# Optimization experiments

Measured on AMD Instinct MI355X. Metric: run time of the kernel, lower is better.

Reference implementation:

```python
import jax, jax.numpy as jnp
import numpy as np
from jax import lax

B, N, C, T = 32, 1000, 32, 24
K, F_CHEB, F_TIME = 3, 64, 64


def setup_inputs() -> dict:
    key = jax.random.key(0)
    ks = jax.random.split(key, 7)
    return {
        "x": jax.random.normal(ks[0], (B, N, C, T), dtype=jnp.float32),
        "cheb_T": jax.random.normal(ks[1], (K, N, N), dtype=jnp.float32) * (1.0 / np.sqrt(N)),
        "Theta": jax.random.normal(ks[2], (K, C, F_CHEB), dtype=jnp.float32) * 0.1,
        "time_w": jax.random.normal(ks[3], (F_TIME, F_CHEB, 1, 3), dtype=jnp.float32) * 0.05,
        "time_b": jax.random.normal(ks[4], (F_TIME,), dtype=jnp.float32) * 0.05,
        "res_w": jax.random.normal(ks[5], (F_TIME, C, 1, 1), dtype=jnp.float32) * 0.1,
        "res_b": jax.random.normal(ks[6], (F_TIME,), dtype=jnp.float32) * 0.05,
    }


def _conv2d(x, w, stride_t, pad_t):
    # x: [B, Cin, N, T] (NCHW with H=nodes, W=time), w: [Cout, Cin, kh, kw]
    return lax.conv_general_dilated(
        x, w, window_strides=(1, stride_t), padding=((0, 0), (pad_t, pad_t)),
        dimension_numbers=("NCHW", "OIHW", "NCHW"))


def reference(x, cheb_T, Theta, time_w, time_b, res_w, res_b):
    # ChebConv: rhs_k[b,n,c,t] = sum_m T_k[m,n] x[b,m,c,t]; out = sum_k rhs_k @ Theta_k
    # Fused over all timesteps and polynomial orders in one einsum.
    spatial = jax.nn.relu(
        jnp.einsum("knm,bmct,kcf->bnft", cheb_T, x, Theta))  # [B,N,F_cheb,T]
    # time conv over the T axis (kernel (1,3), pad (0,1), stride (1,1))
    h = spatial.transpose(0, 2, 1, 3)  # [B,F_cheb,N,T]
    tc = _conv2d(h, time_w, 1, 1) + time_b[None, :, None, None]
    tc = jnp.tanh(tc) * jax.nn.sigmoid(tc)  # wave-net gating
    # 1x1 residual conv on the raw input (Dropout output in source is unused)
    res = _conv2d(x.transpose(0, 2, 1, 3), res_w, 1, 0) + res_b[None, :, None, None]
    out = (res + tc).transpose(0, 2, 1, 3)  # [B,N,F_time,T]
    return out
```

## Files before the change

### kernel.cpp

```cpp
#include <hip/hip_runtime.h>
#include <math.h>

typedef __attribute__((ext_vector_type(4))) float f32x4;
typedef __attribute__((ext_vector_type(16))) float f32x16;
typedef __attribute__((ext_vector_type(8))) short s16x8;
typedef __attribute__((ext_vector_type(8))) unsigned short u16x8;
typedef __attribute__((ext_vector_type(4))) unsigned short u16x4;

#define NB 32
#define NN 1000
#define NT 24
#define NP 1024
#define TCN 768

#define GLOAD16(g, l) __builtin_amdgcn_global_load_lds( \
    (const __attribute__((address_space(1))) unsigned int*)(g), \
    (__attribute__((address_space(3))) unsigned int*)(l), 16, 0, 0)

__device__ __forceinline__ unsigned short f2bf(float f){
  union { float fv; unsigned int u; } v; v.fv = f;
  unsigned int r = v.u + 0x7FFFu + ((v.u >> 16) & 1u);
  return (unsigned short)(r >> 16);
}

__global__ void k0_cheb(const float* __restrict__ cheb, unsigned short* __restrict__ cbT){
  int idx = blockIdx.x * 256 + threadIdx.x;
  int base = idx << 2;
  int m = base & (NP - 1);
  int r = base >> 10;
  int n = r & (NP - 1);
  int k = r >> 10;
  u16x4 o = (u16x4){0,0,0,0};
  if (n < NN && m < NN){
    if (m + 3 < NN){
      f32x4 v = *(const f32x4*)(cheb + ((size_t)k*NN + n)*NN + m);
      o[0] = f2bf(v[0]); o[1] = f2bf(v[1]); o[2] = f2bf(v[2]); o[3] = f2bf(v[3]);
    } else {
      #pragma unroll
      for (int i = 0; i < 4; ++i)
        if (m + i < NN) o[i] = f2bf(cheb[((size_t)k*NN + n)*NN + m + i]);
    }
  }
  *(u16x4*)(cbT + base) = o;
}

__global__ __launch_bounds__(256) void k0_x(const float* __restrict__ x,
                     unsigned short* __restrict__ xbT, unsigned short* __restrict__ xt2){
  __shared__ unsigned short tile[64*770];
  const int b  = blockIdx.x >> 4;
  const int m0 = (blockIdx.x & 15) << 6;
  const int tid = threadIdx.x;
  for (int i = tid; i < 64*192; i += 256){
    int mi = i / 192, c4 = (i - mi*192) << 2;
    f32x4 v = (f32x4){0.f,0.f,0.f,0.f};
    if (m0 + mi < NN) v = *(const f32x4*)(x + (size_t)(b*NN + m0 + mi)*768 + c4);
    unsigned short* tp = tile + mi*770 + c4;
    tp[0] = f2bf(v[0]); tp[1] = f2bf(v[1]); tp[2] = f2bf(v[2]); tp[3] = f2bf(v[3]);
  }
  __syncthreads();
  {
    const int seg = tid & 7, r0 = tid >> 3;
    for (int rr = 0; rr < 768; rr += 32){
      int r = rr + r0;
      int t = r >> 5, c = r & 31, ct = c*24 + t;
      u16x8 v;
      #pragma unroll
      for (int e = 0; e < 8; ++e) v[e] = tile[(seg*8 + e)*770 + ct];
      *(u16x8*)(xbT + ((size_t)b*TCN + r)*NP + m0 + seg*8) = v;
    }
  }
  if (m0 < NN){
    int rows = NN - m0; if (rows > 64) rows = 64;
    for (int i = tid; i < rows*96; i += 256){
      int mi = i / 96, s = i - mi*96;
      u16x8 v;
      #pragma unroll
      for (int e = 0; e < 8; ++e){
        int r = s*8 + e; int t = r >> 5, c = r & 31;
        v[e] = tile[mi*770 + c*24 + t];
      }
      *(u16x8*)(xt2 + (size_t)(b*NN + m0 + mi)*TCN + s*8) = v;
    }
  }
}

__global__ void k0_w(const float* __restrict__ Theta, const float* __restrict__ tw,
                     const float* __restrict__ rw,
                     unsigned short* __restrict__ ThT, unsigned short* __restrict__ WtT,
                     unsigned short* __restrict__ rwT){
  int i = blockIdx.x * 256 + threadIdx.x;
  if (i < 64*96){
    int f = i / 96, kc = i - f*96;
    ThT[i] = f2bf(Theta[kc*64 + f]);
  }
  if (i < 64*192){
    int f = i / 192, kk = i - f*192;
    int dt = kk >> 6, fi = kk & 63;
    WtT[i] = f2bf(tw[(f*64 + fi)*3 + dt]);
  }
  if (i < 64*32){
    rwT[i] = f2bf(rw[i]);
  }
}

__global__ __launch_bounds__(256, 3) void k1_cheb_theta(
    const unsigned short* __restrict__ cbT,
    const unsigned short* __restrict__ xbT,
    const unsigned short* __restrict__ ThT,
    unsigned short* __restrict__ spa)
{
  __shared__ __align__(16) unsigned short smem[20480];

  int pB = blockIdx.x;
  int lb = (pB & 7) * 384 + (pB >> 3);
  const int tcb = lb % 6; lb /= 6;
  const int nt  = lb & 15;
  const int b   = lb >> 4;

  const int tid  = threadIdx.x;
  const int wid  = tid >> 6;
  const int lane = tid & 63;
  const int l31  = lane & 31;
  const int h    = lane >> 5;
  const int wr   = wid >> 1;
  const int wc   = wid & 1;

  const int rl4 = lane >> 2;
  const int swz = (((lane & 3) ^ ((rl4 >> 1) & 3)) << 3);
  const unsigned short* baseA = cbT + (size_t)(nt*64 + rl4)*NP + swz;
  const unsigned short* baseB = xbT + ((size_t)b*TCN + tcb*128 + rl4)*NP + swz;
  char* smc = (char*)smem;

  const int s_rd = (l31 >> 1) & 3;
  const int ch0 = ((h ^ s_rd) << 3);
  const int ch1 = (((2 + h) ^ s_rd) << 3);

  f32x16 acc[3][2];
  #pragma unroll
  for (int k = 0; k < 3; ++k)
    #pragma unroll
    for (int j = 0; j < 2; ++j)
      #pragma unroll
      for (int r = 0; r < 16; ++r) acc[k][j][r] = 0.f;

  const int rA  = wr*32 + l31;
  const int rB0 = wc*64 + l31;

  {
    #pragma unroll
    for (int q = 0; q < 5; ++q){
      const int g = wid*5 + q;
      if (g < 12){
        const int k = g >> 2, rg = g & 3;
        GLOAD16(baseA + (size_t)k*NP*NP + rg*16*NP, smc + k*4096 + rg*1024);
      } else {
        const int rg = g - 12;
        GLOAD16(baseB + (size_t)rg*16*NP, smc + 12288 + rg*1024);
      }
    }
  }
  __syncthreads();

  int cur = 0;
  for (int step = 0; step < 32; ++step){
    if (step < 31){
      const int so = (step + 1) << 5;
      const int bo = (cur ^ 1) * 20480;
      #pragma unroll
      for (int q = 0; q < 5; ++q){
        const int g = wid*5 + q;
        if (g < 12){
          const int k = g >> 2, rg = g & 3;
          GLOAD16(baseA + (size_t)k*NP*NP + rg*16*NP + so, smc + bo + k*4096 + rg*1024);
        } else {
          const int rg = g - 12;
          GLOAD16(baseB + (size_t)rg*16*NP + so, smc + bo + 12288 + rg*1024);
        }
      }
    }
    const unsigned short* sb = smem + cur*10240;
    #pragma unroll
    for (int ks = 0; ks < 2; ++ks){
      const int ch = ks ? ch1 : ch0;
      s16x8 bf0 = *(const s16x8*)(sb + 6144 + rB0*32 + ch);
      s16x8 bf1 = *(const s16x8*)(sb + 6144 + (rB0 + 32)*32 + ch);
      #pragma unroll
      for (int k = 0; k < 3; ++k){
        s16x8 af = *(const s16x8*)(sb + k*2048 + rA*32 + ch);
        acc[k][0] = __builtin_amdgcn_mfma_f32_32x32x16_bf16(af, bf0, acc[k][0], 0, 0, 0);
        acc[k][1] = __builtin_amdgcn_mfma_f32_32x32x16_bf16(af, bf1, acc[k][1], 0, 0, 0);
      }
    }
    __syncthreads();
    cur ^= 1;
  }

  s16x8 b2[3][2];
  const int fE = wc*32 + l31;
  #pragma unroll
  for (int ch = 0; ch < 3; ++ch)
    #pragma unroll
    for (int ks = 0; ks < 2; ++ks)
      b2[ch][ks] = *(const s16x8*)(ThT + fE*96 + ch*32 + ks*16 + h*8);

  unsigned short* yl = smem;
  const int rowE = wr*32 + l31;
  #pragma unroll
  for (int p = 0; p < 4; ++p){
    __syncthreads();
    if (wc == (p >> 1)){
      const int jj = p & 1;
      #pragma unroll
      for (int k = 0; k < 3; ++k)
        #pragma unroll
        for (int r = 0; r < 16; ++r){
          const int nl = wr*32 + (r & 3) + ((r >> 2) << 3) + (h << 2);
          const int kc = k*32 + l31;
          const int q  = kc >> 3;
          yl[nl*104 + (((q ^ (nl & 3)) << 3) | (kc & 7))] = f2bf(acc[k][jj][r]);
        }
    }
    __syncthreads();
    f32x16 a2c;
    #pragma unroll
    for (int r = 0; r < 16; ++r) a2c[r] = 0.f;
    #pragma unroll
    for (int ch = 0; ch < 3; ++ch)
      #pragma unroll
      for (int ks = 0; ks < 2; ++ks){
        const int q = ch*4 + ks*2 + h;
        s16x8 a2 = *(const s16x8*)(yl + rowE*104 + ((q ^ (rowE & 3)) << 3));
        a2c = __builtin_amdgcn_mfma_f32_32x32x16_bf16(a2, b2[ch][ks], a2c, 0, 0, 0);
      }
    const int t = tcb*4 + p;
    #pragma unroll
    for (int r = 0; r < 16; ++r){
      const int nl = wr*32 + (r & 3) + ((r >> 2) << 3) + (h << 2);
      const int n  = nt*64 + nl;
      if (n < NN)
        spa[((size_t)(b*NN + n)*NT + t)*64 + fE] = f2bf(fmaxf(a2c[r], 0.f));
    }
  }
}

__global__ __launch_bounds__(256, 2) void k2_out(
    const unsigned short* __restrict__ spa, const unsigned short* __restrict__ xt2,
    const unsigned short* __restrict__ WtT, const unsigned short* __restrict__ rwT,
    const float* __restrict__ tb, const float* __restrict__ rb,
    float* __restrict__ out)
{
  __shared__ __align__(16) unsigned short sst[36864];
  const unsigned short* spa_s = sst;
  const unsigned short* xt2_s = sst + 24576;

  const int c0   = blockIdx.x * 16;
  const int tid  = threadIdx.x;
  const int w    = tid >> 6;
  const int lane = tid & 63;
  const int l31  = lane & 31;
  const int h    = lane >> 5;
  char* smc = (char*)sst;

  const unsigned short* gs = spa + (size_t)c0 * 1536;
  const unsigned short* gx = xt2 + (size_t)c0 * 768;
  #pragma unroll
  for (int it = 0; it < 12; ++it){
    const int row = it*32 + (tid >> 3);
    const int sc  = (tid & 7) ^ (row & 7);
    GLOAD16(gs + (size_t)row*64 + sc*8, smc + it*4096 + w*1024);
  }
  #pragma unroll
  for (int it = 0; it < 6; ++it){
    const int row = it*64 + (tid >> 2);
    const int sc  = (tid & 3) ^ ((row >> 1) & 3);
    GLOAD16(gx + (size_t)row*32 + sc*8, smc + 49152 + it*4096 + w*1024);
  }
  __syncthreads();

  const float tb0v = tb[l31], tb1v = tb[32 + l31];
  const float rb0v = rb[l31], rb1v = rb[32 + l31];

  #pragma unroll
  for (int g = 0; g < 3; ++g){
    const int rbase = w*96 + g*32;
    const int r = rbase + l31;
    const int cell = r / 24;
    const int t = r - cell*24;

    f32x16 a0, a1, rs0, rs1;
    #pragma unroll
    for (int e = 0; e < 16; ++e){ a0[e]=0.f; a1[e]=0.f; rs0[e]=0.f; rs1[e]=0.f; }

    #pragma unroll
    for (int s = 0; s < 12; ++s){
      const int dt = s >> 2;
      const int tv = t + dt - 1;
      int ar = r + dt - 1;
      ar = ar < 0 ? 0 : (ar > 383 ? 383 : ar);
      const int cfi = ((s & 3) << 1) + h;
      s16x8 a = *(const s16x8*)(spa_s + (size_t)ar*64 + ((cfi ^ (ar & 7)) << 3));
      if (!((unsigned)tv < 24u)) a = (s16x8){0,0,0,0,0,0,0,0};
      s16x8 b0 = *(const s16x8*)(WtT + (size_t)l31*192 + s*16 + h*8);
      s16x8 b1 = *(const s16x8*)(WtT + (size_t)(32 + l31)*192 + s*16 + h*8);
      a0 = __builtin_amdgcn_mfma_f32_32x32x16_bf16(a, b0, a0, 0, 0, 0);
      a1 = __builtin_amdgcn_mfma_f32_32x32x16_bf16(a, b1, a1, 0, 0, 0);
    }
    #pragma unroll
    for (int s = 0; s < 2; ++s){
      const int cres = (s << 1) + h;
      s16x8 a = *(const s16x8*)(xt2_s + (size_t)r*32 + ((cres ^ ((r >> 1) & 3)) << 3));
      s16x8 b0 = *(const s16x8*)(rwT + (size_t)l31*32 + s*16 + h*8);
      s16x8 b1 = *(const s16x8*)(rwT + (size_t)(32 + l31)*32 + s*16 + h*8);
      rs0 = __builtin_amdgcn_mfma_f32_32x32x16_bf16(a, b0, rs0, 0, 0, 0);
      rs1 = __builtin_amdgcn_mfma_f32_32x32x16_bf16(a, b1, rs1, 0, 0, 0);
    }

    #pragma unroll
    for (int q = 0; q < 4; ++q){
      const int rq = rbase + q*8 + 4*h;
      const int cq = rq / 24;
      const int tq = rq - cq*24;
      f32x4 v0, v1;
      #pragma unroll
      for (int e = 0; e < 4; ++e){
        float z0 = a0[q*4 + e] + tb0v;
        float e0 = __expf(-z0);
        v0[e] = rs0[q*4 + e] + rb0v + (1.f - e0) * __builtin_amdgcn_rcpf(1.f + e0*e0);
        float z1 = a1[q*4 + e] + tb1v;
        float e1 = __expf(-z1);
        v1[e] = rs1[q*4 + e] + rb1v + (1.f - e1) * __builtin_amdgcn_rcpf(1.f + e1*e1);
      }
      *(f32x4*)(out + ((size_t)(c0 + cq)*64 + l31)*24 + tq)      = v0;
      *(f32x4*)(out + ((size_t)(c0 + cq)*64 + 32 + l31)*24 + tq) = v1;
    }
  }
}

extern "C" void kernel_launch(void* const* d_in, const int* in_sizes, int n_in,
                              void* d_out, int out_size, void* d_ws, size_t ws_size,
                              hipStream_t stream) {
  const float* x     = (const float*)d_in[0];
  const float* cheb  = (const float*)d_in[1];
  const float* Theta = (const float*)d_in[2];
  const float* tw    = (const float*)d_in[3];
  const float* tb    = (const float*)d_in[4];
  const float* rw    = (const float*)d_in[5];
  const float* rb    = (const float*)d_in[6];
  float* out = (float*)d_out;

  char* ws = (char*)d_ws;
  size_t off = 0;
  auto alloc = [&](size_t bytes) -> void* {
    void* p = ws + off;
    off += (bytes + 255) & ~(size_t)255;
    return p;
  };
  unsigned short* cbT = (unsigned short*)alloc((size_t)3*NP*NP*2);
  unsigned short* xbT = (unsigned short*)alloc((size_t)NB*TCN*NP*2);
  unsigned short* xt2 = (unsigned short*)alloc((size_t)NB*NN*TCN*2);
  unsigned short* spa = (unsigned short*)alloc((size_t)NB*NN*NT*64*2);
  unsigned short* ThT = (unsigned short*)alloc((size_t)64*96*2);
  unsigned short* WtT = (unsigned short*)alloc((size_t)64*192*2);
  unsigned short* rwT = (unsigned short*)alloc((size_t)64*32*2);

  hipLaunchKernelGGL(k0_cheb, dim3(3072), dim3(256), 0, stream, cheb, cbT);
  hipLaunchKernelGGL(k0_x,    dim3(512),  dim3(256), 0, stream, x, xbT, xt2);
  hipLaunchKernelGGL(k0_w,    dim3(48),   dim3(256), 0, stream, Theta, tw, rw, ThT, WtT, rwT);
  hipLaunchKernelGGL(k1_cheb_theta, dim3(32*16*6), dim3(256), 0, stream, cbT, xbT, ThT, spa);
  hipLaunchKernelGGL(k2_out,  dim3(2000), dim3(256), 0, stream, spa, xt2, WtT, rwT, tb, rb, out);
}
```

Before: 391.8 us.

## Triple-buffer k1 loads with explicit vmcnt waits and MFMA priority

Extends the k1 GEMM main loop from double to triple buffering in LDS, so loads are prefetched two steps ahead. The previous __syncthreads is replaced by explicit s_waitcnt vmcnt plus s_barrier, which lets one stage's loads stay in flight across the barrier. MFMAs are grouped after hoisting the A-fragment LDS reads and wrapped in s_setprio. The larger LDS footprint lowers the launch-bounds occupancy target from 3 to 2 blocks per CU, trading latency hiding from occupancy for deeper prefetch.

```diff
diff --git a/kernel.cpp b/kernel.cpp
--- a/kernel.cpp
+++ b/kernel.cpp
@@ -103,13 +103,13 @@
   }
 }
 
-__global__ __launch_bounds__(256, 3) void k1_cheb_theta(
+__global__ __launch_bounds__(256, 2) void k1_cheb_theta(
     const unsigned short* __restrict__ cbT,
     const unsigned short* __restrict__ xbT,
     const unsigned short* __restrict__ ThT,
     unsigned short* __restrict__ spa)
 {
-  __shared__ __align__(16) unsigned short smem[20480];
+  __shared__ __align__(16) unsigned short smem[30720];
 
   int pB = blockIdx.x;
   int lb = (pB & 7) * 384 + (pB >> 3);
@@ -146,53 +146,53 @@
   const int rA  = wr*32 + l31;
   const int rB0 = wc*64 + l31;
 
-  {
+  auto stage = [&](int step, int buf){
+    const int so = step << 5;
+    const int bo = buf * 20480;
     #pragma unroll
     for (int q = 0; q < 5; ++q){
       const int g = wid*5 + q;
       if (g < 12){
         const int k = g >> 2, rg = g & 3;
-        GLOAD16(baseA + (size_t)k*NP*NP + rg*16*NP, smc + k*4096 + rg*1024);
+        GLOAD16(baseA + (size_t)k*NP*NP + rg*16*NP + so, smc + bo + k*4096 + rg*1024);
       } else {
         const int rg = g - 12;
-        GLOAD16(baseB + (size_t)rg*16*NP, smc + 12288 + rg*1024);
+        GLOAD16(baseB + (size_t)rg*16*NP + so, smc + bo + 12288 + rg*1024);
       }
     }
-  }
-  __syncthreads();
-
-  int cur = 0;
+  };
+
+  stage(0, 0);
+  stage(1, 1);
+  asm volatile("s_waitcnt vmcnt(5)" ::: "memory");
+  __builtin_amdgcn_s_barrier();
+
+  int cur = 0, pre = 2;
   for (int step = 0; step < 32; ++step){
-    if (step < 31){
-      const int so = (step + 1) << 5;
-      const int bo = (cur ^ 1) * 20480;
-      #pragma unroll
-      for (int q = 0; q < 5; ++q){
-        const int g = wid*5 + q;
-        if (g < 12){
-          const int k = g >> 2, rg = g & 3;
-          GLOAD16(baseA + (size_t)k*NP*NP + rg*16*NP + so, smc + bo + k*4096 + rg*1024);
-        } else {
-          const int rg = g - 12;
-          GLOAD16(baseB + (size_t)rg*16*NP + so, smc + bo + 12288 + rg*1024);
-        }
-      }
-    }
+    if (step < 30) stage(step + 2, pre);
     const unsigned short* sb = smem + cur*10240;
     #pragma unroll
     for (int ks = 0; ks < 2; ++ks){
       const int ch = ks ? ch1 : ch0;
       s16x8 bf0 = *(const s16x8*)(sb + 6144 + rB0*32 + ch);
       s16x8 bf1 = *(const s16x8*)(sb + 6144 + (rB0 + 32)*32 + ch);
-      #pragma unroll
-      for (int k = 0; k < 3; ++k){
-        s16x8 af = *(const s16x8*)(sb + k*2048 + rA*32 + ch);
-        acc[k][0] = __builtin_amdgcn_mfma_f32_32x32x16_bf16(af, bf0, acc[k][0], 0, 0, 0);
-        acc[k][1] = __builtin_amdgcn_mfma_f32_32x32x16_bf16(af, bf1, acc[k][1], 0, 0, 0);
-      }
-    }
-    __syncthreads();
-    cur ^= 1;
+      s16x8 af0 = *(const s16x8*)(sb +        rA*32 + ch);
+      s16x8 af1 = *(const s16x8*)(sb + 2048 + rA*32 + ch);
+      s16x8 af2 = *(const s16x8*)(sb + 4096 + rA*32 + ch);
+      __builtin_amdgcn_s_setprio(1);
+      acc[0][0] = __builtin_amdgcn_mfma_f32_32x32x16_bf16(af0, bf0, acc[0][0], 0, 0, 0);
+      acc[0][1] = __builtin_amdgcn_mfma_f32_32x32x16_bf16(af0, bf1, acc[0][1], 0, 0, 0);
+      acc[1][0] = __builtin_amdgcn_mfma_f32_32x32x16_bf16(af1, bf0, acc[1][0], 0, 0, 0);
+      acc[1][1] = __builtin_amdgcn_mfma_f32_32x32x16_bf16(af1, bf1, acc[1][1], 0, 0, 0);
+      acc[2][0] = __builtin_amdgcn_mfma_f32_32x32x16_bf16(af2, bf0, acc[2][0], 0, 0, 0);
+      acc[2][1] = __builtin_amdgcn_mfma_f32_32x32x16_bf16(af2, bf1, acc[2][1], 0, 0, 0);
+      __builtin_amdgcn_s_setprio(0);
+    }
+    if (step < 30)       asm volatile("s_waitcnt vmcnt(5)" ::: "memory");
+    else if (step == 30) asm volatile("s_waitcnt vmcnt(0)" ::: "memory");
+    __builtin_amdgcn_s_barrier();
+    cur = (cur == 2) ? 0 : cur + 1;
+    pre = (pre == 2) ? 0 : pre + 1;
   }
 
   s16x8 b2[3][2];
```

After: 396.4 us. About the same (+1.2%).

## Load B operand directly from global into registers, shrink LDS, reorder block mapping

Applied to the files above, without the earlier changes.

The B (x) operand of the Chebyshev GEMM no longer goes through LDS. Each wave reads its MFMA fragments straight from global memory into registers, prefetching one step ahead, while only the three cheb_T A tiles are staged in LDS. This shrinks LDS per block and cuts LDS write and read traffic. The block-index decomposition also changes so that node tiles vary fastest, meant to improve L2 reuse of the x tiles across blocks. In exchange there are more per-thread global loads with less coalescing, plus extra register pressure.

```diff
diff --git a/kernel.cpp b/kernel.cpp
--- a/kernel.cpp
+++ b/kernel.cpp
@@ -109,13 +109,13 @@
     const unsigned short* __restrict__ ThT,
     unsigned short* __restrict__ spa)
 {
-  __shared__ __align__(16) unsigned short smem[20480];
+  __shared__ __align__(16) unsigned short smem[12288];
 
   int pB = blockIdx.x;
   int lb = (pB & 7) * 384 + (pB >> 3);
-  const int tcb = lb % 6; lb /= 6;
-  const int nt  = lb & 15;
-  const int b   = lb >> 4;
+  const int nt  = lb & 15; lb >>= 4;
+  const int tcb = lb % 6;
+  const int b   = lb / 6;
 
   const int tid  = threadIdx.x;
   const int wid  = tid >> 6;
@@ -128,7 +128,6 @@
   const int rl4 = lane >> 2;
   const int swz = (((lane & 3) ^ ((rl4 >> 1) & 3)) << 3);
   const unsigned short* baseA = cbT + (size_t)(nt*64 + rl4)*NP + swz;
-  const unsigned short* baseB = xbT + ((size_t)b*TCN + tcb*128 + rl4)*NP + swz;
   char* smc = (char*)smem;
 
   const int s_rd = (l31 >> 1) & 3;
@@ -143,54 +142,62 @@
       #pragma unroll
       for (int r = 0; r < 16; ++r) acc[k][j][r] = 0.f;
 
-  const int rA  = wr*32 + l31;
-  const int rB0 = wc*64 + l31;
-
-  {
-    #pragma unroll
-    for (int q = 0; q < 5; ++q){
-      const int g = wid*5 + q;
-      if (g < 12){
-        const int k = g >> 2, rg = g & 3;
-        GLOAD16(baseA + (size_t)k*NP*NP + rg*16*NP, smc + k*4096 + rg*1024);
-      } else {
-        const int rg = g - 12;
-        GLOAD16(baseB + (size_t)rg*16*NP, smc + 12288 + rg*1024);
-      }
-    }
-  }
+  const int rA = wr*32 + l31;
+  const unsigned short* gBF = xbT + ((size_t)b*TCN + tcb*128 + wc*64 + l31)*NP + h*8;
+
+  auto stage = [&](int step, int buf){
+    const int so = step << 5;
+    const int bo = buf * 12288;
+    #pragma unroll
+    for (int q = 0; q < 3; ++q){
+      const int g = wid*3 + q;
+      const int k = g >> 2, rg = g & 3;
+      GLOAD16(baseA + (size_t)k*NP*NP + rg*16*NP + so, smc + bo + k*4096 + rg*1024);
+    }
+  };
+
+  stage(0, 0);
+  s16x8 c00 = *(const s16x8*)(gBF);
+  s16x8 c01 = *(const s16x8*)(gBF + 16);
+  s16x8 c10 = *(const s16x8*)(gBF + 32*NP);
+  s16x8 c11 = *(const s16x8*)(gBF + 32*NP + 16);
   __syncthreads();
 
   int cur = 0;
   for (int step = 0; step < 32; ++step){
+    s16x8 n00, n01, n10, n11;
     if (step < 31){
+      stage(step + 1, cur ^ 1);
       const int so = (step + 1) << 5;
-      const int bo = (cur ^ 1) * 20480;
-      #pragma unroll
-      for (int q = 0; q < 5; ++q){
-        const int g = wid*5 + q;
-        if (g < 12){
-          const int k = g >> 2, rg = g & 3;
-          GLOAD16(baseA + (size_t)k*NP*NP + rg*16*NP + so, smc + bo + k*4096 + rg*1024);
-        } else {
-          const int rg = g - 12;
-          GLOAD16(baseB + (size_t)rg*16*NP + so, smc + bo + 12288 + rg*1024);
-        }
-      }
-    }
-    const unsigned short* sb = smem + cur*10240;
-    #pragma unroll
-    for (int ks = 0; ks < 2; ++ks){
-      const int ch = ks ? ch1 : ch0;
-      s16x8 bf0 = *(const s16x8*)(sb + 6144 + rB0*32 + ch);
-      s16x8 bf1 = *(const s16x8*)(sb + 6144 + (rB0 + 32)*32 + ch);
-      #pragma unroll
-      for (int k = 0; k < 3; ++k){
-        s16x8 af = *(const s16x8*)(sb + k*2048 + rA*32 + ch);
-        acc[k][0] = __builtin_amdgcn_mfma_f32_32x32x16_bf16(af, bf0, acc[k][0], 0, 0, 0);
-        acc[k][1] = __builtin_amdgcn_mfma_f32_32x32x16_bf16(af, bf1, acc[k][1], 0, 0, 0);
-      }
-    }
+      n00 = *(const s16x8*)(gBF + so);
+      n01 = *(const s16x8*)(gBF + so + 16);
+      n10 = *(const s16x8*)(gBF + 32*NP + so);
+      n11 = *(const s16x8*)(gBF + 32*NP + so + 16);
+    }
+    const unsigned short* sb = smem + cur*6144;
+    {
+      s16x8 af0 = *(const s16x8*)(sb +        rA*32 + ch0);
+      s16x8 af1 = *(const s16x8*)(sb + 2048 + rA*32 + ch0);
+      s16x8 af2 = *(const s16x8*)(sb + 4096 + rA*32 + ch0);
+      acc[0][0] = __builtin_amdgcn_mfma_f32_32x32x16_bf16(af0, c00, acc[0][0], 0, 0, 0);
+      acc[0][1] = __builtin_amdgcn_mfma_f32_32x32x16_bf16(af0, c10, acc[0][1], 0, 0, 0);
+      acc[1][0] = __builtin_amdgcn_mfma_f32_32x32x16_bf16(af1, c00, acc[1][0], 0, 0, 0);
+      acc[1][1] = __builtin_amdgcn_mfma_f32_32x32x16_bf16(af1, c10, acc[1][1], 0, 0, 0);
+      acc[2][0] = __builtin_amdgcn_mfma_f32_32x32x16_bf16(af2, c00, acc[2][0], 0, 0, 0);
+      acc[2][1] = __builtin_amdgcn_mfma_f32_32x32x16_bf16(af2, c10, acc[2][1], 0, 0, 0);
+    }
+    {
+      s16x8 af0 = *(const s16x8*)(sb +        rA*32 + ch1);
+      s16x8 af1 = *(const s16x8*)(sb + 2048 + rA*32 + ch1);
+      s16x8 af2 = *(const s16x8*)(sb + 4096 + rA*32 + ch1);
+      acc[0][0] = __builtin_amdgcn_mfma_f32_32x32x16_bf16(af0, c01, acc[0][0], 0, 0, 0);
+      acc[0][1] = __builtin_amdgcn_mfma_f32_32x32x16_bf16(af0, c11, acc[0][1], 0, 0, 0);
+      acc[1][0] = __builtin_amdgcn_mfma_f32_32x32x16_bf16(af1, c01, acc[1][0], 0, 0, 0);
+      acc[1][1] = __builtin_amdgcn_mfma_f32_32x32x16_bf16(af1, c11, acc[1][1], 0, 0, 0);
+      acc[2][0] = __builtin_amdgcn_mfma_f32_32x32x16_bf16(af2, c01, acc[2][0], 0, 0, 0);
+      acc[2][1] = __builtin_amdgcn_mfma_f32_32x32x16_bf16(af2, c11, acc[2][1], 0, 0, 0);
+    }
+    c00 = n00; c01 = n01; c10 = n10; c11 = n11;
     __syncthreads();
     cur ^= 1;
   }
```

New measurement: 445.8 us. 1.14x slower.
